# Kernel tuning notes

Hardware: AMD Instinct MI355X
Metric: run time of the kernel (lower is better)

## Reference

```python
import jax, jax.numpy as jnp
import numpy as np

N = 20000
E = 320000
F_IN = 256
NHID = 64
H1 = 8
H2 = 1
NUM_CLASSES = 40
NEG_SLOPE = 0.2


def setup_inputs() -> dict:
    key = jax.random.key(0)
    ks = jax.random.split(key, 11)
    glorot = lambda k, shape: jax.random.normal(k, shape, jnp.float32) * jnp.sqrt(2.0 / (shape[0] + shape[-1]))
    x = jax.random.normal(ks[0], (N, F_IN), jnp.float32)
    edge_index = jax.random.randint(ks[1], (2, E), 0, N, jnp.int64)
    W1 = glorot(ks[2], (F_IN, H1 * NHID))
    att_src1 = glorot(ks[3], (H1, NHID))
    att_dst1 = glorot(ks[4], (H1, NHID))
    b1 = jnp.zeros((H1 * NHID,), jnp.float32)
    W2 = glorot(ks[5], (H1 * NHID, H2 * NUM_CLASSES))
    att_src2 = glorot(ks[6], (H2, NUM_CLASSES))
    att_dst2 = glorot(ks[7], (H2, NUM_CLASSES))
    b2 = jnp.zeros((NUM_CLASSES,), jnp.float32)
    return {"x": x, "edge_index": edge_index, "W1": W1, "att_src1": att_src1,
            "att_dst1": att_dst1, "b1": b1, "W2": W2, "att_src2": att_src2,
            "att_dst2": att_dst2, "b2": b2}


def gat_conv(x, src, dst, W, a_src, a_dst, bias, concat):
    # x: [N, F_in], src/dst: [E'] (self-loops already appended)
    H, C = a_src.shape
    h = (x @ W).reshape(N, H, C)                       # [N,H,C]
    alpha_src = jnp.sum(h * a_src, axis=-1)            # [N,H]
    alpha_dst = jnp.sum(h * a_dst, axis=-1)            # [N,H]
    e = jax.nn.leaky_relu(alpha_src[src] + alpha_dst[dst], NEG_SLOPE)  # [E',H]
    # segment softmax over incoming edges of each dst node
    emax = jax.lax.stop_gradient(jax.ops.segment_max(e, dst, num_segments=N))
    ee = jnp.exp(e - emax[dst])
    denom = jax.ops.segment_sum(ee, dst, num_segments=N)
    alpha = ee / (denom[dst] + 1e-16)                  # [E',H]
    out = jax.ops.segment_sum(alpha[:, :, None] * h[src], dst, num_segments=N)  # [N,H,C]
    out = out.reshape(N, H * C) if concat else out.mean(axis=1)
    return out + bias


def reference(x, edge_index, W1, att_src1, att_dst1, b1, W2, att_src2, att_dst2, b2):
    # PyG GATConv adds self-loops by default
    loops = jnp.arange(N, dtype=edge_index.dtype)
    src = jnp.concatenate([edge_index[0], loops])
    dst = jnp.concatenate([edge_index[1], loops])
    h = gat_conv(x, src, dst, W1, att_src1, att_dst1, b1, concat=True)   # [N, H1*NHID]
    h = jax.nn.elu(h)
    out = gat_conv(h, src, dst, W2, att_src2, att_dst2, b2, concat=False)  # [N, NUM_CLASSES]
    return jax.nn.log_softmax(out, axis=1)
```

## Files before the change

kernel.cpp:

```cpp
#include <hip/hip_runtime.h>
#include <hip/hip_bf16.h>
#include <math.h>

#define N_NODES 20000
#define MPAD 20096
#define N_EDGES 320000
#define EP (N_EDGES + N_NODES)
#define F_IN 256
#define NHID 64
#define H1 8
#define D1 512
#define NCLS 40
#define NEG_SLOPE 0.2f
#define MAXD 128

typedef __attribute__((ext_vector_type(8))) short bf16x8;
typedef __attribute__((ext_vector_type(4))) float f32x4;

__device__ __forceinline__ float wave_max(float v) {
#pragma unroll
  for (int o = 32; o > 0; o >>= 1) v = fmaxf(v, __shfl_xor(v, o));
  return v;
}
__device__ __forceinline__ float wave_sum(float v) {
#pragma unroll
  for (int o = 32; o > 0; o >>= 1) v += __shfl_xor(v, o);
  return v;
}
__device__ __forceinline__ float bf2f(unsigned short u) {
  union { unsigned int i; float f; } c; c.i = ((unsigned int)u) << 16; return c.f;
}
__device__ __forceinline__ unsigned short f2bf(float f) {
  union { float f; unsigned int i; } c; c.f = f;
  unsigned int x = c.i;
  return (unsigned short)((x + 0x7fffu + ((x >> 16) & 1u)) >> 16);
}
__device__ __forceinline__ float asf(unsigned int u) {
  union { unsigned int i; float f; } c; c.i = u; return c.f;
}
__device__ __forceinline__ float lrelu(float x) { return x > 0.f ? x : NEG_SLOPE * x; }

__device__ __forceinline__ void gload16(const void* g, void* l) {
  __builtin_amdgcn_global_load_lds((const __attribute__((address_space(1))) void*)g,
                                   (__attribute__((address_space(3))) void*)l, 16, 0, 0);
}

#define PB_CONV 2512
#define PB_TW1  (PB_CONV + 32)
#define PB_TW2  (PB_TW1 + 96)
#define PB_ZERO (PB_TW2 + 157)
#define PB_PAD  (PB_ZERO + 24)
__global__ __launch_bounds__(256) void prep_kernel(const float* __restrict__ x,
                                                   const float* __restrict__ W1,
                                                   const float* __restrict__ W2,
                                                   unsigned short* __restrict__ xb,
                                                   unsigned short* __restrict__ wb1t,
                                                   unsigned short* __restrict__ wb2t,
                                                   int* __restrict__ deg,
                                                   int* __restrict__ cursor,
                                                   unsigned short* __restrict__ out1b) {
  __shared__ float tsh[64][65];
  int bid = blockIdx.x;
  int t = threadIdx.x;
  if (bid < PB_CONV) {
    size_t base = ((size_t)bid * 256 + t) * 8;
    int row = (int)(base >> 8);
    ushort4 o0, o1;
    if (row < N_NODES) {
      float4 v0 = *(const float4*)&x[base];
      float4 v1 = *(const float4*)&x[base + 4];
      o0 = make_ushort4(f2bf(v0.x), f2bf(v0.y), f2bf(v0.z), f2bf(v0.w));
      o1 = make_ushort4(f2bf(v1.x), f2bf(v1.y), f2bf(v1.z), f2bf(v1.w));
    } else {
      o0 = make_ushort4(0, 0, 0, 0); o1 = o0;
    }
    *(ushort4*)&xb[base] = o0;
    *(ushort4*)&xb[base + 4] = o1;
  } else if (bid < PB_TW1) {
    int b2 = bid - PB_CONV;
    int bk = b2 & 3, bn = b2 >> 2;
    int tr = t >> 4, tc4 = (t & 15) * 4;
#pragma unroll
    for (int i = 0; i < 4; ++i) {
      int k = i * 16 + tr;
      float4 v = *(const float4*)&W1[(size_t)(bk * 64 + k) * D1 + bn * 64 + tc4];
      tsh[k][tc4] = v.x; tsh[k][tc4 + 1] = v.y; tsh[k][tc4 + 2] = v.z; tsh[k][tc4 + 3] = v.w;
    }
    __syncthreads();
#pragma unroll
    for (int i = 0; i < 4; ++i) {
      int n = i * 16 + tr;
      ushort4 o = make_ushort4(f2bf(tsh[tc4][n]), f2bf(tsh[tc4 + 1][n]),
                               f2bf(tsh[tc4 + 2][n]), f2bf(tsh[tc4 + 3][n]));
      *(ushort4*)&wb1t[(size_t)(bn * 64 + n) * F_IN + bk * 64 + tc4] = o;
    }
  } else if (bid < PB_TW2) {
    int idx = (bid - PB_TW1) * 256 + t;
    int c = idx >> 9, k = idx & 511;
    wb2t[idx] = f2bf((c < NCLS) ? W2[(size_t)k * NCLS + c] : 0.f);
  } else if (bid < PB_ZERO) {
    int idx = (bid - PB_TW2) * 256 + t;
    if (idx < N_NODES) deg[idx] = 0;
    else if (idx < 2 * N_NODES) cursor[idx - N_NODES] = 0;
  } else {
    int idx = (bid - PB_ZERO) * 256 + t;
    uint4 z = make_uint4(0, 0, 0, 0);
    *(uint4*)((char*)out1b + (size_t)N_NODES * D1 * 2 + (size_t)idx * 16) = z;
  }
}

__global__ void count_deg(const int* __restrict__ ei, int* __restrict__ deg) {
  int e = blockIdx.x * blockDim.x + threadIdx.x;
  if (e >= EP) return;
  int dst = (e < N_EDGES) ? ei[N_EDGES + e] : (e - N_EDGES);
  atomicAdd(&deg[dst], 1);
}

#define SCAN_T 1024
#define SCAN_CHUNK 20
__global__ __launch_bounds__(1024) void scan_kernel(const int* __restrict__ deg,
                                                    int* __restrict__ offsets) {
  __shared__ int wsum[16];
  int t = threadIdx.x;
  int w = t >> 6, lane = t & 63;
  int lo = t * SCAN_CHUNK;
  int hi = min(lo + SCAN_CHUNK, N_NODES);
  int s = 0;
  for (int i = lo; i < hi; ++i) s += deg[i];
  int incl = s;
#pragma unroll
  for (int o = 1; o < 64; o <<= 1) {
    int v = __shfl_up(incl, o);
    if (lane >= o) incl += v;
  }
  if (lane == 63) wsum[w] = incl;
  __syncthreads();
  if (t == 0) {
    int run = 0;
#pragma unroll
    for (int i = 0; i < 16; ++i) { int v = wsum[i]; wsum[i] = run; run += v; }
  }
  __syncthreads();
  int off = wsum[w] + incl - s;
  for (int i = lo; i < hi; ++i) { offsets[i] = off; off += deg[i]; }
  if (hi == N_NODES && lo < N_NODES) offsets[N_NODES] = off;
}

__global__ void scatter_edges(const int* __restrict__ ei, const int* __restrict__ offsets,
                              int* __restrict__ cursor, int* __restrict__ edge_src) {
  int e = blockIdx.x * blockDim.x + threadIdx.x;
  if (e >= EP) return;
  int src, dst;
  if (e < N_EDGES) { src = ei[e]; dst = ei[N_EDGES + e]; }
  else             { src = dst = e - N_EDGES; }
  int pos = offsets[dst] + atomicAdd(&cursor[dst], 1);
  edge_src[pos] = src;
}

__global__ __launch_bounds__(256) void gemm1_mfma(const unsigned short* __restrict__ xb,
                                                  const unsigned short* __restrict__ wb1t,
                                                  const float* __restrict__ a_src,
                                                  const float* __restrict__ a_dst,
                                                  unsigned short* __restrict__ h1b,
                                                  float* __restrict__ asrc,
                                                  float* __restrict__ adst) {
  __shared__ unsigned short As[128 * 64];
  __shared__ unsigned short Bs[128 * 64];
  int tid = threadIdx.x;
  int w = tid >> 6, lane = tid & 63;
  int bn = blockIdx.x & 3, bm = blockIdx.x >> 2;
  int row0 = bm * 128, col0 = bn * 128;
  int wr = w >> 1, wc = w & 1;
  int cl = lane & 15, hi = lane >> 4;
  f32x4 acc[4][4] = {};
  for (int k0 = 0; k0 < F_IN; k0 += 64) {
#pragma unroll
    for (int c = 0; c < 4; ++c) {
      int slot = c * 256 + tid;
      int r = slot >> 3;
      int q = (slot & 7) ^ (r & 7);
      gload16(xb + (size_t)(row0 + r) * F_IN + k0 + q * 8, (char*)As + (c * 256 + w * 64) * 16);
      gload16(wb1t + (size_t)(col0 + r) * F_IN + k0 + q * 8, (char*)Bs + (c * 256 + w * 64) * 16);
    }
    __syncthreads();
#pragma unroll
    for (int kk = 0; kk < 2; ++kk) {
      bf16x8 a[4], b[4];
#pragma unroll
      for (int m = 0; m < 4; ++m) {
        int r = wr * 64 + m * 16 + cl;
        a[m] = *(const bf16x8*)&As[r * 64 + ((((kk * 4 + hi)) ^ (r & 7)) << 3)];
      }
#pragma unroll
      for (int n = 0; n < 4; ++n) {
        int r = wc * 64 + n * 16 + cl;
        b[n] = *(const bf16x8*)&Bs[r * 64 + ((((kk * 4 + hi)) ^ (r & 7)) << 3)];
      }
#pragma unroll
      for (int m = 0; m < 4; ++m)
#pragma unroll
        for (int n = 0; n < 4; ++n)
          acc[m][n] = __builtin_amdgcn_mfma_f32_16x16x32_bf16(a[m], b[n], acc[m][n], 0, 0, 0);
    }
    __syncthreads();
  }
  int head = bn * 2 + wc;
  float asv[4], adv[4];
#pragma unroll
  for (int n = 0; n < 4; ++n) {
    asv[n] = a_src[head * 64 + n * 16 + cl];
    adv[n] = a_dst[head * 64 + n * 16 + cl];
  }
#pragma unroll
  for (int m = 0; m < 4; ++m) {
#pragma unroll
    for (int r = 0; r < 4; ++r) {
      int grow = row0 + wr * 64 + m * 16 + hi * 4 + r;
      float ps = acc[m][0][r] * asv[0] + acc[m][1][r] * asv[1] +
                 acc[m][2][r] * asv[2] + acc[m][3][r] * asv[3];
      float pd = acc[m][0][r] * adv[0] + acc[m][1][r] * adv[1] +
                 acc[m][2][r] * adv[2] + acc[m][3][r] * adv[3];
#pragma unroll
      for (int o = 8; o > 0; o >>= 1) { ps += __shfl_xor(ps, o); pd += __shfl_xor(pd, o); }
      if (grow < N_NODES) {
#pragma unroll
        for (int n = 0; n < 4; ++n)
          h1b[(size_t)grow * D1 + col0 + wc * 64 + n * 16 + cl] = f2bf(acc[m][n][r]);
        if (cl == 0) { asrc[grow * H1 + head] = ps; adst[grow * H1 + head] = pd; }
      }
    }
  }
}

__global__ __launch_bounds__(256) void agg1_kernel(const int* __restrict__ offsets,
                                                   const int* __restrict__ edge_src,
                                                   const float* __restrict__ asrc,
                                                   const float* __restrict__ adst,
                                                   const unsigned short* __restrict__ h1b,
                                                   const float* __restrict__ b1,
                                                   unsigned short* __restrict__ out1b) {
  __shared__ float alphaT[4][MAXD][H1];
  __shared__ int   lsoff[4][MAXD];
  int w = threadIdx.x >> 6, lane = threadIdx.x & 63;
  int n = blockIdx.x * 4 + w;
  int base = offsets[n];
  int deg = offsets[n + 1] - base;
  int degc = min(deg, MAXD);

  for (int e = lane; e < degc; e += 64) lsoff[w][e] = edge_src[base + e] << 10;
  __builtin_amdgcn_wave_barrier();

  int h = lane & 7, et = lane >> 3;
  float advv = adst[n * H1 + h];
  float m = -INFINITY;
  for (int e = et; e < degc; e += 8) {
    int s = lsoff[w][e] >> 10;
    float ev = lrelu(asrc[s * H1 + h] + advv);
    alphaT[w][e][h] = ev;
    m = fmaxf(m, ev);
  }
  for (int e = MAXD + et; e < deg; e += 8)
    m = fmaxf(m, lrelu(asrc[edge_src[base + e] * H1 + h] + advv));
  m = fmaxf(m, __shfl_xor(m, 8));
  m = fmaxf(m, __shfl_xor(m, 16));
  m = fmaxf(m, __shfl_xor(m, 32));
  float ss = 0.f;
  for (int e = et; e < degc; e += 8) ss += __expf(alphaT[w][e][h] - m);
  for (int e = MAXD + et; e < deg; e += 8)
    ss += __expf(lrelu(asrc[edge_src[base + e] * H1 + h] + advv) - m);
  ss += __shfl_xor(ss, 8);
  ss += __shfl_xor(ss, 16);
  ss += __shfl_xor(ss, 32);
  float inv = 1.f / (ss + 1e-16f);
  for (int e = et; e < degc; e += 8)
    alphaT[w][e][h] = __expf(alphaT[w][e][h] - m) * inv;
  __builtin_amdgcn_wave_barrier();

  int myh = lane >> 3;
  const char* hb = (const char*)h1b + lane * 16;
  float acc[8] = {};
  int e = 0;
  for (; e + 1 < degc; e += 2) {
    float a0 = alphaT[w][e][myh];
    float a1 = alphaT[w][e + 1][myh];
    uint4 u0 = *(const uint4*)(hb + lsoff[w][e]);
    uint4 u1 = *(const uint4*)(hb + lsoff[w][e + 1]);
#pragma unroll
    for (int j = 0; j < 4; ++j) {
      unsigned int x0 = ((const unsigned int*)&u0)[j];
      unsigned int x1 = ((const unsigned int*)&u1)[j];
      acc[2 * j]     += a0 * asf(x0 << 16);
      acc[2 * j + 1] += a0 * asf(x0 & 0xffff0000u);
      acc[2 * j]     += a1 * asf(x1 << 16);
      acc[2 * j + 1] += a1 * asf(x1 & 0xffff0000u);
    }
  }
  for (; e < degc; ++e) {
    float a = alphaT[w][e][myh];
    uint4 uv = *(const uint4*)(hb + lsoff[w][e]);
#pragma unroll
    for (int j = 0; j < 4; ++j) {
      unsigned int u = ((const unsigned int*)&uv)[j];
      acc[2 * j]     += a * asf(u << 16);
      acc[2 * j + 1] += a * asf(u & 0xffff0000u);
    }
  }
  if (deg > MAXD) {
    float mh = __shfl(m, myh);
    float invh = __shfl(inv, myh);
    float advh = adst[n * H1 + myh];
    for (int e2 = MAXD; e2 < deg; ++e2) {
      int s = edge_src[base + e2];
      float a = __expf(lrelu(asrc[s * H1 + myh] + advh) - mh) * invh;
      uint4 uv = *(const uint4*)(hb + ((size_t)s << 10));
#pragma unroll
      for (int j = 0; j < 4; ++j) {
        unsigned int u = ((const unsigned int*)&uv)[j];
        acc[2 * j]     += a * asf(u << 16);
        acc[2 * j + 1] += a * asf(u & 0xffff0000u);
      }
    }
  }

  int c0 = lane * 8;
  float4 b0 = *(const float4*)&b1[c0];
  float4 b4 = *(const float4*)&b1[c0 + 4];
  float v[8];
  v[0] = acc[0] + b0.x; v[1] = acc[1] + b0.y; v[2] = acc[2] + b0.z; v[3] = acc[3] + b0.w;
  v[4] = acc[4] + b4.x; v[5] = acc[5] + b4.y; v[6] = acc[6] + b4.z; v[7] = acc[7] + b4.w;
#pragma unroll
  for (int j = 0; j < 8; ++j) v[j] = v[j] > 0.f ? v[j] : (__expf(v[j]) - 1.f);
  ushort4 o0 = make_ushort4(f2bf(v[0]), f2bf(v[1]), f2bf(v[2]), f2bf(v[3]));
  ushort4 o1 = make_ushort4(f2bf(v[4]), f2bf(v[5]), f2bf(v[6]), f2bf(v[7]));
  *(ushort4*)&out1b[(size_t)n * D1 + c0] = o0;
  *(ushort4*)&out1b[(size_t)n * D1 + c0 + 4] = o1;
}

__global__ __launch_bounds__(256) void gemm2_mfma(const unsigned short* __restrict__ ab,
                                                  const unsigned short* __restrict__ wb2t,
                                                  const float* __restrict__ a_src2,
                                                  const float* __restrict__ a_dst2,
                                                  float* __restrict__ h2,
                                                  float* __restrict__ asrc,
                                                  float* __restrict__ adst) {
  __shared__ unsigned short As[64 * 64];
  __shared__ unsigned short Bs[48 * 64];
  int tid = threadIdx.x;
  int w = tid >> 6, lane = tid & 63;
  int row0 = blockIdx.x * 64;
  int cl = lane & 15, hi = lane >> 4;
  f32x4 acc[3] = {};
  for (int k0 = 0; k0 < D1; k0 += 64) {
#pragma unroll
    for (int c = 0; c < 2; ++c) {
      int slot = c * 256 + tid;
      int r = slot >> 3;
      int q = (slot & 7) ^ (r & 7);
      gload16(ab + (size_t)(row0 + r) * D1 + k0 + q * 8, (char*)As + (c * 256 + w * 64) * 16);
    }
    {
      int r = tid >> 3;
      int q = (tid & 7) ^ (r & 7);
      gload16(wb2t + (size_t)r * D1 + k0 + q * 8, (char*)Bs + (w * 64) * 16);
      if (tid < 128) {
        int slot2 = 256 + tid;
        int r2 = slot2 >> 3;
        int q2 = (slot2 & 7) ^ (r2 & 7);
        gload16(wb2t + (size_t)r2 * D1 + k0 + q2 * 8, (char*)Bs + ((256 + w * 64)) * 16);
      }
    }
    __syncthreads();
#pragma unroll
    for (int kk = 0; kk < 2; ++kk) {
      int ra = w * 16 + cl;
      bf16x8 a = *(const bf16x8*)&As[ra * 64 + (((kk * 4 + hi) ^ (ra & 7)) << 3)];
#pragma unroll
      for (int n = 0; n < 3; ++n) {
        int rb = n * 16 + cl;
        bf16x8 b = *(const bf16x8*)&Bs[rb * 64 + (((kk * 4 + hi) ^ (rb & 7)) << 3)];
        acc[n] = __builtin_amdgcn_mfma_f32_16x16x32_bf16(a, b, acc[n], 0, 0, 0);
      }
    }
    __syncthreads();
  }
  float asv[3], adv[3];
#pragma unroll
  for (int n = 0; n < 3; ++n) {
    int c = n * 16 + cl;
    asv[n] = (c < NCLS) ? a_src2[c] : 0.f;
    adv[n] = (c < NCLS) ? a_dst2[c] : 0.f;
  }
#pragma unroll
  for (int r = 0; r < 4; ++r) {
    int grow = row0 + w * 16 + hi * 4 + r;
    float ps = acc[0][r] * asv[0] + acc[1][r] * asv[1] + acc[2][r] * asv[2];
    float pd = acc[0][r] * adv[0] + acc[1][r] * adv[1] + acc[2][r] * adv[2];
#pragma unroll
    for (int o = 8; o > 0; o >>= 1) { ps += __shfl_xor(ps, o); pd += __shfl_xor(pd, o); }
    if (grow < N_NODES) {
#pragma unroll
      for (int n = 0; n < 3; ++n) {
        int c = n * 16 + cl;
        if (c < NCLS) h2[(size_t)grow * NCLS + c] = acc[n][r];
      }
      if (cl == 0) { asrc[grow] = ps; adst[grow] = pd; }
    }
  }
}

__global__ __launch_bounds__(256) void agg2_kernel(const int* __restrict__ offsets,
                                                   const int* __restrict__ edge_src,
                                                   const float* __restrict__ asrc,
                                                   const float* __restrict__ adst,
                                                   const float* __restrict__ h2,
                                                   const float* __restrict__ b2,
                                                   float* __restrict__ out) {
  __shared__ float lalpha[4][MAXD];
  __shared__ int   lsoff[4][MAXD];
  int w = threadIdx.x >> 6;
  int lane = threadIdx.x & 63;
  int n = blockIdx.x * 4 + w;
  int base = offsets[n];
  int deg = offsets[n + 1] - base;
  int degc = min(deg, MAXD);
  int degp = ((degc + 2) / 3) * 3;

  float advv = adst[n];
  float m = -INFINITY;
  for (int e = lane; e < deg; e += 64) {
    int s = edge_src[base + e];
    float ev = lrelu(asrc[s] + advv);
    if (e < MAXD) { lsoff[w][e] = s * (NCLS * 4); lalpha[w][e] = ev; }
    m = fmaxf(m, ev);
  }
  m = wave_max(m);
  float ssum = 0.f;
  for (int e = lane; e < deg; e += 64) {
    float ev;
    if (e < MAXD) ev = lalpha[w][e];
    else { int s = edge_src[base + e]; ev = lrelu(asrc[s] + advv); }
    ssum += __expf(ev - m);
  }
  float inv = 1.f / (wave_sum(ssum) + 1e-16f);
  for (int e = lane; e < degc; e += 64) lalpha[w][e] = __expf(lalpha[w][e] - m) * inv;
  {
    int e = degc + lane;
    if (e < degp && e < MAXD) { lalpha[w][e] = 0.f; lsoff[w][e] = 0; }
  }
  __builtin_amdgcn_wave_barrier();

  int esub = lane / 20;
  int cg = lane - esub * 20;
  bool act = esub < 3;
  float ax = 0.f, ay = 0.f;
  const char* hb = (const char*)h2 + cg * 8;
  for (int i = 0; i < degp; i += 3) {
    if (act) {
      int slot = i + esub;
      float a = lalpha[w][slot];
      int so = lsoff[w][slot];
      float2 hv = *(const float2*)(hb + so);
      ax += a * hv.x; ay += a * hv.y;
    }
  }
  for (int e = MAXD + esub; e < deg; e += 3) {
    if (act) {
      int s = edge_src[base + e];
      float a = __expf(lrelu(asrc[s] + advv) - m) * inv;
      float2 hv = *(const float2*)(hb + (size_t)s * (NCLS * 4));
      ax += a * hv.x; ay += a * hv.y;
    }
  }
  float ax1 = __shfl(ax, lane + 20), ax2 = __shfl(ax, lane + 40);
  float ay1 = __shfl(ay, lane + 20), ay2 = __shfl(ay, lane + 40);
  float v0 = -INFINITY, v1 = -INFINITY;
  if (lane < 20) {
    v0 = ax + ax1 + ax2 + b2[2 * cg];
    v1 = ay + ay1 + ay2 + b2[2 * cg + 1];
  }
  float m2 = wave_max(fmaxf(v0, v1));
  float se = wave_sum(lane < 20 ? __expf(v0 - m2) + __expf(v1 - m2) : 0.f);
  if (lane < 20) {
    float ls = logf(se);
    *(float2*)&out[(size_t)n * NCLS + 2 * cg] = make_float2(v0 - m2 - ls, v1 - m2 - ls);
  }
}

extern "C" void kernel_launch(void* const* d_in, const int* in_sizes, int n_in,
                              void* d_out, int out_size, void* d_ws, size_t ws_size,
                              hipStream_t stream) {
  const float* x   = (const float*)d_in[0];
  const int*   ei  = (const int*)d_in[1];
  const float* W1  = (const float*)d_in[2];
  const float* as1 = (const float*)d_in[3];
  const float* ad1 = (const float*)d_in[4];
  const float* b1  = (const float*)d_in[5];
  const float* W2  = (const float*)d_in[6];
  const float* as2 = (const float*)d_in[7];
  const float* ad2 = (const float*)d_in[8];
  const float* b2  = (const float*)d_in[9];
  float* out = (float*)d_out;

  char* ws = (char*)d_ws;
  size_t off = 0;
  auto alloc = [&](size_t bytes) -> char* {
    char* p = ws + off;
    off += (bytes + 255) & ~(size_t)255;
    return p;
  };
  int* deg      = (int*)alloc((size_t)N_NODES * 4);
  int* cursor   = (int*)alloc((size_t)N_NODES * 4);
  int* offsets  = (int*)alloc((size_t)(N_NODES + 1) * 4);
  int* edge_src = (int*)alloc((size_t)EP * 4);
  unsigned short* xb    = (unsigned short*)alloc((size_t)MPAD * F_IN * 2);
  unsigned short* wb1t  = (unsigned short*)alloc((size_t)D1 * F_IN * 2);
  unsigned short* wb2t  = (unsigned short*)alloc((size_t)48 * D1 * 2);
  unsigned short* h1b   = (unsigned short*)alloc((size_t)N_NODES * D1 * 2);
  unsigned short* out1b = (unsigned short*)alloc((size_t)MPAD * D1 * 2);
  float* asrc1  = (float*)alloc((size_t)N_NODES * H1 * 4);
  float* adst1  = (float*)alloc((size_t)N_NODES * H1 * 4);
  float* h2     = (float*)alloc((size_t)N_NODES * NCLS * 4);
  float* asrc2  = (float*)alloc((size_t)N_NODES * 4);
  float* adst2  = (float*)alloc((size_t)N_NODES * 4);

  prep_kernel<<<PB_PAD, 256, 0, stream>>>(x, W1, W2, xb, wb1t, wb2t, deg, cursor, out1b);
  count_deg<<<(EP + 255) / 256, 256, 0, stream>>>(ei, deg);
  scan_kernel<<<1, SCAN_T, 0, stream>>>(deg, offsets);
  scatter_edges<<<(EP + 255) / 256, 256, 0, stream>>>(ei, offsets, cursor, edge_src);

  gemm1_mfma<<<157 * 4, 256, 0, stream>>>(xb, wb1t, as1, ad1, h1b, asrc1, adst1);
  agg1_kernel<<<N_NODES / 4, 256, 0, stream>>>(offsets, edge_src, asrc1, adst1, h1b, b1, out1b);

  gemm2_mfma<<<MPAD / 64, 256, 0, stream>>>(out1b, wb2t, as2, ad2, h2, asrc2, adst2);
  agg2_kernel<<<N_NODES / 4, 256, 0, stream>>>(offsets, edge_src, asrc2, adst2, h2, b2, out);
}
```

Measured before the change: 159.3 us.

## Split layer-1 aggregation across heads with one wave per node-head pair

The layer-1 aggregation kernel now launches eight times more blocks, and each wave handles a single (node, head) pair instead of all eight heads of one node. Softmax values for up to 64 edges live in registers and are broadcast with shuffles, which replaces the shared-memory alpha and offset tables. The gather processes four edges at a time with 8-byte loads per lane, followed by a cross-lane reduction. This raises parallelism and removes LDS use, at the cost of re-reading offsets, edge_src and asrc once per head, issuing narrower gather loads, and leaving most lanes idle for low-degree nodes.

After: 192.2 us. +20.6%, slower.

```diff
diff --git a/kernel.cpp b/kernel.cpp
--- a/kernel.cpp
+++ b/kernel.cpp
@@ -239,101 +239,71 @@
                                                    const unsigned short* __restrict__ h1b,
                                                    const float* __restrict__ b1,
                                                    unsigned short* __restrict__ out1b) {
-  __shared__ float alphaT[4][MAXD][H1];
-  __shared__ int   lsoff[4][MAXD];
   int w = threadIdx.x >> 6, lane = threadIdx.x & 63;
-  int n = blockIdx.x * 4 + w;
+  int bid = blockIdx.x;
+  int head = bid & 7;
+  int n = (bid >> 3) * 4 + w;
   int base = offsets[n];
   int deg = offsets[n + 1] - base;
-  int degc = min(deg, MAXD);
-
-  for (int e = lane; e < degc; e += 64) lsoff[w][e] = edge_src[base + e] << 10;
-  __builtin_amdgcn_wave_barrier();
-
-  int h = lane & 7, et = lane >> 3;
-  float advv = adst[n * H1 + h];
-  float m = -INFINITY;
-  for (int e = et; e < degc; e += 8) {
-    int s = lsoff[w][e] >> 10;
-    float ev = lrelu(asrc[s * H1 + h] + advv);
-    alphaT[w][e][h] = ev;
-    m = fmaxf(m, ev);
-  }
-  for (int e = MAXD + et; e < deg; e += 8)
-    m = fmaxf(m, lrelu(asrc[edge_src[base + e] * H1 + h] + advv));
-  m = fmaxf(m, __shfl_xor(m, 8));
-  m = fmaxf(m, __shfl_xor(m, 16));
-  m = fmaxf(m, __shfl_xor(m, 32));
-  float ss = 0.f;
-  for (int e = et; e < degc; e += 8) ss += __expf(alphaT[w][e][h] - m);
-  for (int e = MAXD + et; e < deg; e += 8)
-    ss += __expf(lrelu(asrc[edge_src[base + e] * H1 + h] + advv) - m);
-  ss += __shfl_xor(ss, 8);
-  ss += __shfl_xor(ss, 16);
-  ss += __shfl_xor(ss, 32);
-  float inv = 1.f / (ss + 1e-16f);
-  for (int e = et; e < degc; e += 8)
-    alphaT[w][e][h] = __expf(alphaT[w][e][h] - m) * inv;
-  __builtin_amdgcn_wave_barrier();
-
-  int myh = lane >> 3;
-  const char* hb = (const char*)h1b + lane * 16;
-  float acc[8] = {};
-  int e = 0;
-  for (; e + 1 < degc; e += 2) {
-    float a0 = alphaT[w][e][myh];
-    float a1 = alphaT[w][e + 1][myh];
-    uint4 u0 = *(const uint4*)(hb + lsoff[w][e]);
-    uint4 u1 = *(const uint4*)(hb + lsoff[w][e + 1]);
-#pragma unroll
-    for (int j = 0; j < 4; ++j) {
-      unsigned int x0 = ((const unsigned int*)&u0)[j];
-      unsigned int x1 = ((const unsigned int*)&u1)[j];
-      acc[2 * j]     += a0 * asf(x0 << 16);
-      acc[2 * j + 1] += a0 * asf(x0 & 0xffff0000u);
-      acc[2 * j]     += a1 * asf(x1 << 16);
-      acc[2 * j + 1] += a1 * asf(x1 & 0xffff0000u);
-    }
-  }
-  for (; e < degc; ++e) {
-    float a = alphaT[w][e][myh];
-    uint4 uv = *(const uint4*)(hb + lsoff[w][e]);
-#pragma unroll
-    for (int j = 0; j < 4; ++j) {
-      unsigned int u = ((const unsigned int*)&uv)[j];
-      acc[2 * j]     += a * asf(u << 16);
-      acc[2 * j + 1] += a * asf(u & 0xffff0000u);
-    }
-  }
-  if (deg > MAXD) {
-    float mh = __shfl(m, myh);
-    float invh = __shfl(inv, myh);
-    float advh = adst[n * H1 + myh];
-    for (int e2 = MAXD; e2 < deg; ++e2) {
-      int s = edge_src[base + e2];
-      float a = __expf(lrelu(asrc[s * H1 + myh] + advh) - mh) * invh;
-      uint4 uv = *(const uint4*)(hb + ((size_t)s << 10));
-#pragma unroll
-      for (int j = 0; j < 4; ++j) {
-        unsigned int u = ((const unsigned int*)&uv)[j];
-        acc[2 * j]     += a * asf(u << 16);
-        acc[2 * j + 1] += a * asf(u & 0xffff0000u);
-      }
-    }
-  }
-
-  int c0 = lane * 8;
-  float4 b0 = *(const float4*)&b1[c0];
-  float4 b4 = *(const float4*)&b1[c0 + 4];
-  float v[8];
-  v[0] = acc[0] + b0.x; v[1] = acc[1] + b0.y; v[2] = acc[2] + b0.z; v[3] = acc[3] + b0.w;
-  v[4] = acc[4] + b4.x; v[5] = acc[5] + b4.y; v[6] = acc[6] + b4.z; v[7] = acc[7] + b4.w;
-#pragma unroll
-  for (int j = 0; j < 8; ++j) v[j] = v[j] > 0.f ? v[j] : (__expf(v[j]) - 1.f);
-  ushort4 o0 = make_ushort4(f2bf(v[0]), f2bf(v[1]), f2bf(v[2]), f2bf(v[3]));
-  ushort4 o1 = make_ushort4(f2bf(v[4]), f2bf(v[5]), f2bf(v[6]), f2bf(v[7]));
-  *(ushort4*)&out1b[(size_t)n * D1 + c0] = o0;
-  *(ushort4*)&out1b[(size_t)n * D1 + c0 + 4] = o1;
+
+  float adv = adst[n * H1 + head];
+  int src = 0;
+  float ev = -INFINITY;
+  if (lane < deg) {
+    src = edge_src[base + lane];
+    ev = lrelu(asrc[src * H1 + head] + adv);
+  }
+  float mx = -INFINITY;
+  for (int e = 64 + lane; e < deg; e += 64)
+    mx = fmaxf(mx, lrelu(asrc[edge_src[base + e] * H1 + head] + adv));
+  float m = wave_max(fmaxf(ev, mx));
+  float ssl = (lane < deg) ? __expf(ev - m) : 0.f;
+  for (int e = 64 + lane; e < deg; e += 64)
+    ssl += __expf(lrelu(asrc[edge_src[base + e] * H1 + head] + adv) - m);
+  float inv = 1.f / (wave_sum(ssl) + 1e-16f);
+  float alpha = (lane < deg) ? __expf(ev - m) * inv : 0.f;
+  int rowoff = src << 10;
+
+  int eg = lane >> 4, cl = lane & 15;
+  const char* hb = (const char*)h1b + head * 128 + cl * 8;
+  float a0 = 0.f, a1 = 0.f, a2 = 0.f, a3 = 0.f;
+  int dc = min(deg, 64);
+  for (int e0 = 0; e0 < dc; e0 += 4) {
+    int e = e0 + eg;
+    int esafe = (e < dc) ? e : 0;
+    float a = __shfl(alpha, esafe);
+    int ro = __shfl(rowoff, esafe);
+    if (e >= dc) a = 0.f;
+    uint2 uv = *(const uint2*)(hb + ro);
+    a0 += a * asf(uv.x << 16);
+    a1 += a * asf(uv.x & 0xffff0000u);
+    a2 += a * asf(uv.y << 16);
+    a3 += a * asf(uv.y & 0xffff0000u);
+  }
+  for (int e = 64 + eg; e < deg; e += 4) {
+    int s2 = edge_src[base + e];
+    float a = __expf(lrelu(asrc[s2 * H1 + head] + adv) - m) * inv;
+    uint2 uv = *(const uint2*)(hb + ((size_t)s2 << 10));
+    a0 += a * asf(uv.x << 16);
+    a1 += a * asf(uv.x & 0xffff0000u);
+    a2 += a * asf(uv.y << 16);
+    a3 += a * asf(uv.y & 0xffff0000u);
+  }
+  a0 += __shfl_xor(a0, 16); a0 += __shfl_xor(a0, 32);
+  a1 += __shfl_xor(a1, 16); a1 += __shfl_xor(a1, 32);
+  a2 += __shfl_xor(a2, 16); a2 += __shfl_xor(a2, 32);
+  a3 += __shfl_xor(a3, 16); a3 += __shfl_xor(a3, 32);
+  if (lane < 16) {
+    int c0 = head * NHID + cl * 4;
+    float4 bv = *(const float4*)&b1[c0];
+    float v0 = a0 + bv.x, v1 = a1 + bv.y, v2 = a2 + bv.z, v3 = a3 + bv.w;
+    v0 = v0 > 0.f ? v0 : (__expf(v0) - 1.f);
+    v1 = v1 > 0.f ? v1 : (__expf(v1) - 1.f);
+    v2 = v2 > 0.f ? v2 : (__expf(v2) - 1.f);
+    v3 = v3 > 0.f ? v3 : (__expf(v3) - 1.f);
+    ushort4 o = make_ushort4(f2bf(v0), f2bf(v1), f2bf(v2), f2bf(v3));
+    *(ushort4*)&out1b[(size_t)n * D1 + c0] = o;
+  }
 }
 
 __global__ __launch_bounds__(256) void gemm2_mfma(const unsigned short* __restrict__ ab,
@@ -529,7 +499,7 @@
   scatter_edges<<<(EP + 255) / 256, 256, 0, stream>>>(ei, offsets, cursor, edge_src);
 
   gemm1_mfma<<<157 * 4, 256, 0, stream>>>(xb, wb1t, as1, ad1, h1b, asrc1, adst1);
-  agg1_kernel<<<N_NODES / 4, 256, 0, stream>>>(offsets, edge_src, asrc1, adst1, h1b, b1, out1b);
+  agg1_kernel<<<(N_NODES / 4) * 8, 256, 0, stream>>>(offsets, edge_src, asrc1, adst1, h1b, b1, out1b);
 
   gemm2_mfma<<<MPAD / 64, 256, 0, stream>>>(out1b, wb2t, as2, ad2, h2, asrc2, adst2);
   agg2_kernel<<<N_NODES / 4, 256, 0, stream>>>(offsets, edge_src, asrc2, adst2, h2, b2, out);
```

## Split layer-1 aggregation into per-edge alpha kernel and head-parallel gather

Applied to the files above, without the earlier changes.

Layer-1 aggregation is split in two. A new kernel computes the unnormalized attention exponentials per edge and head, writes them to a head-major global array, and stores each node's inverse softmax sum. A second kernel gathers features with one 8-lane group per node and one head per block, so blocks grouped by head touch a 128-byte slice of h1 rows, and normalization moves to the epilogue. This drops the LDS staging and the MAXD special path, but adds an extra launch and a global round trip for roughly 11 MB of alpha values. It also reloads edge_src once per head.

Result: no change. 162.5 us (+2.0%).

```diff
diff --git a/kernel.cpp b/kernel.cpp
--- a/kernel.cpp
+++ b/kernel.cpp
@@ -26,9 +26,6 @@
 #pragma unroll
   for (int o = 32; o > 0; o >>= 1) v += __shfl_xor(v, o);
   return v;
-}
-__device__ __forceinline__ float bf2f(unsigned short u) {
-  union { unsigned int i; float f; } c; c.i = ((unsigned int)u) << 16; return c.f;
 }
 __device__ __forceinline__ unsigned short f2bf(float f) {
   union { float f; unsigned int i; } c; c.f = f;
@@ -232,72 +229,91 @@
   }
 }
 
-__global__ __launch_bounds__(256) void agg1_kernel(const int* __restrict__ offsets,
-                                                   const int* __restrict__ edge_src,
-                                                   const float* __restrict__ asrc,
-                                                   const float* __restrict__ adst,
-                                                   const unsigned short* __restrict__ h1b,
-                                                   const float* __restrict__ b1,
-                                                   unsigned short* __restrict__ out1b) {
-  __shared__ float alphaT[4][MAXD][H1];
-  __shared__ int   lsoff[4][MAXD];
+__global__ __launch_bounds__(256) void alpha1_kernel(const int* __restrict__ offsets,
+                                                     const int* __restrict__ edge_src,
+                                                     const float* __restrict__ asrc,
+                                                     const float* __restrict__ adst,
+                                                     float* __restrict__ alphaE,
+                                                     float* __restrict__ inv1) {
   int w = threadIdx.x >> 6, lane = threadIdx.x & 63;
   int n = blockIdx.x * 4 + w;
   int base = offsets[n];
   int deg = offsets[n + 1] - base;
-  int degc = min(deg, MAXD);
-
-  for (int e = lane; e < degc; e += 64) lsoff[w][e] = edge_src[base + e] << 10;
-  __builtin_amdgcn_wave_barrier();
-
   int h = lane & 7, et = lane >> 3;
-  float advv = adst[n * H1 + h];
+  float adv = adst[n * H1 + h];
+  float evr[8];
   float m = -INFINITY;
-  for (int e = et; e < degc; e += 8) {
-    int s = lsoff[w][e] >> 10;
-    float ev = lrelu(asrc[s * H1 + h] + advv);
-    alphaT[w][e][h] = ev;
+#pragma unroll
+  for (int k = 0; k < 8; ++k) {
+    int e = et + k * 8;
+    float ev = -INFINITY;
+    if (e < deg) ev = lrelu(asrc[edge_src[base + e] * H1 + h] + adv);
+    evr[k] = ev;
     m = fmaxf(m, ev);
   }
-  for (int e = MAXD + et; e < deg; e += 8)
-    m = fmaxf(m, lrelu(asrc[edge_src[base + e] * H1 + h] + advv));
+  for (int e = et + 64; e < deg; e += 8)
+    m = fmaxf(m, lrelu(asrc[edge_src[base + e] * H1 + h] + adv));
   m = fmaxf(m, __shfl_xor(m, 8));
   m = fmaxf(m, __shfl_xor(m, 16));
   m = fmaxf(m, __shfl_xor(m, 32));
   float ss = 0.f;
-  for (int e = et; e < degc; e += 8) ss += __expf(alphaT[w][e][h] - m);
-  for (int e = MAXD + et; e < deg; e += 8)
-    ss += __expf(lrelu(asrc[edge_src[base + e] * H1 + h] + advv) - m);
+#pragma unroll
+  for (int k = 0; k < 8; ++k) {
+    int e = et + k * 8;
+    if (e < deg) {
+      float a = __expf(evr[k] - m);
+      alphaE[(size_t)h * EP + base + e] = a;
+      ss += a;
+    }
+  }
+  for (int e = et + 64; e < deg; e += 8) {
+    float a = __expf(lrelu(asrc[edge_src[base + e] * H1 + h] + adv) - m);
+    alphaE[(size_t)h * EP + base + e] = a;
+    ss += a;
+  }
   ss += __shfl_xor(ss, 8);
   ss += __shfl_xor(ss, 16);
   ss += __shfl_xor(ss, 32);
-  float inv = 1.f / (ss + 1e-16f);
-  for (int e = et; e < degc; e += 8)
-    alphaT[w][e][h] = __expf(alphaT[w][e][h] - m) * inv;
-  __builtin_amdgcn_wave_barrier();
-
-  int myh = lane >> 3;
-  const char* hb = (const char*)h1b + lane * 16;
+  if (et == 0) inv1[n * H1 + h] = 1.f / (ss + 1e-16f);
+}
+
+__global__ __launch_bounds__(256) void agg1_gather(const int* __restrict__ offsets,
+                                                   const int* __restrict__ edge_src,
+                                                   const float* __restrict__ alphaE,
+                                                   const float* __restrict__ inv1,
+                                                   const unsigned short* __restrict__ h1b,
+                                                   const float* __restrict__ b1,
+                                                   unsigned short* __restrict__ out1b) {
+  int w = threadIdx.x >> 6, lane = threadIdx.x & 63;
+  int bid = blockIdx.x;
+  int head = bid & 7;
+  int ng = bid >> 3;
+  int sub = lane >> 3, cl = lane & 7;
+  int n = ng * 32 + w * 8 + sub;
+  int base = offsets[n];
+  int deg = offsets[n + 1] - base;
+  const float* aE = alphaE + (size_t)head * EP + base;
+  const int* es = edge_src + base;
+  const char* hb = (const char*)h1b + head * 128 + cl * 16;
   float acc[8] = {};
   int e = 0;
-  for (; e + 1 < degc; e += 2) {
-    float a0 = alphaT[w][e][myh];
-    float a1 = alphaT[w][e + 1][myh];
-    uint4 u0 = *(const uint4*)(hb + lsoff[w][e]);
-    uint4 u1 = *(const uint4*)(hb + lsoff[w][e + 1]);
+  for (; e + 1 < deg; e += 2) {
+    float a0 = aE[e], a1 = aE[e + 1];
+    int s0 = es[e], s1 = es[e + 1];
+    uint4 u0 = *(const uint4*)(hb + ((size_t)s0 << 10));
+    uint4 u1 = *(const uint4*)(hb + ((size_t)s1 << 10));
 #pragma unroll
     for (int j = 0; j < 4; ++j) {
       unsigned int x0 = ((const unsigned int*)&u0)[j];
       unsigned int x1 = ((const unsigned int*)&u1)[j];
-      acc[2 * j]     += a0 * asf(x0 << 16);
-      acc[2 * j + 1] += a0 * asf(x0 & 0xffff0000u);
-      acc[2 * j]     += a1 * asf(x1 << 16);
-      acc[2 * j + 1] += a1 * asf(x1 & 0xffff0000u);
-    }
-  }
-  for (; e < degc; ++e) {
-    float a = alphaT[w][e][myh];
-    uint4 uv = *(const uint4*)(hb + lsoff[w][e]);
+      acc[2 * j]     += a0 * asf(x0 << 16) + a1 * asf(x1 << 16);
+      acc[2 * j + 1] += a0 * asf(x0 & 0xffff0000u) + a1 * asf(x1 & 0xffff0000u);
+    }
+  }
+  if (e < deg) {
+    float a = aE[e];
+    int s = es[e];
+    uint4 uv = *(const uint4*)(hb + ((size_t)s << 10));
 #pragma unroll
     for (int j = 0; j < 4; ++j) {
       unsigned int u = ((const unsigned int*)&uv)[j];
@@ -305,29 +321,15 @@
       acc[2 * j + 1] += a * asf(u & 0xffff0000u);
     }
   }
-  if (deg > MAXD) {
-    float mh = __shfl(m, myh);
-    float invh = __shfl(inv, myh);
-    float advh = adst[n * H1 + myh];
-    for (int e2 = MAXD; e2 < deg; ++e2) {
-      int s = edge_src[base + e2];
-      float a = __expf(lrelu(asrc[s * H1 + myh] + advh) - mh) * invh;
-      uint4 uv = *(const uint4*)(hb + ((size_t)s << 10));
-#pragma unroll
-      for (int j = 0; j < 4; ++j) {
-        unsigned int u = ((const unsigned int*)&uv)[j];
-        acc[2 * j]     += a * asf(u << 16);
-        acc[2 * j + 1] += a * asf(u & 0xffff0000u);
-      }
-    }
-  }
-
-  int c0 = lane * 8;
+  float inv = inv1[n * H1 + head];
+  int c0 = head * NHID + cl * 8;
   float4 b0 = *(const float4*)&b1[c0];
   float4 b4 = *(const float4*)&b1[c0 + 4];
   float v[8];
-  v[0] = acc[0] + b0.x; v[1] = acc[1] + b0.y; v[2] = acc[2] + b0.z; v[3] = acc[3] + b0.w;
-  v[4] = acc[4] + b4.x; v[5] = acc[5] + b4.y; v[6] = acc[6] + b4.z; v[7] = acc[7] + b4.w;
+  v[0] = acc[0] * inv + b0.x; v[1] = acc[1] * inv + b0.y;
+  v[2] = acc[2] * inv + b0.z; v[3] = acc[3] * inv + b0.w;
+  v[4] = acc[4] * inv + b4.x; v[5] = acc[5] * inv + b4.y;
+  v[6] = acc[6] * inv + b4.z; v[7] = acc[7] * inv + b4.w;
 #pragma unroll
   for (int j = 0; j < 8; ++j) v[j] = v[j] > 0.f ? v[j] : (__expf(v[j]) - 1.f);
   ushort4 o0 = make_ushort4(f2bf(v[0]), f2bf(v[1]), f2bf(v[2]), f2bf(v[3]));
@@ -519,6 +521,8 @@
   unsigned short* out1b = (unsigned short*)alloc((size_t)MPAD * D1 * 2);
   float* asrc1  = (float*)alloc((size_t)N_NODES * H1 * 4);
   float* adst1  = (float*)alloc((size_t)N_NODES * H1 * 4);
+  float* alphaE = (float*)alloc((size_t)H1 * EP * 4);
+  float* inv1   = (float*)alloc((size_t)N_NODES * H1 * 4);
   float* h2     = (float*)alloc((size_t)N_NODES * NCLS * 4);
   float* asrc2  = (float*)alloc((size_t)N_NODES * 4);
   float* adst2  = (float*)alloc((size_t)N_NODES * 4);
@@ -529,7 +533,8 @@
   scatter_edges<<<(EP + 255) / 256, 256, 0, stream>>>(ei, offsets, cursor, edge_src);
 
   gemm1_mfma<<<157 * 4, 256, 0, stream>>>(xb, wb1t, as1, ad1, h1b, asrc1, adst1);
-  agg1_kernel<<<N_NODES / 4, 256, 0, stream>>>(offsets, edge_src, asrc1, adst1, h1b, b1, out1b);
+  alpha1_kernel<<<N_NODES / 4, 256, 0, stream>>>(offsets, edge_src, asrc1, adst1, alphaE, inv1);
+  agg1_gather<<<(N_NODES / 32) * 8, 256, 0, stream>>>(offsets, edge_src, alphaE, inv1, h1b, b1, out1b);
 
   gemm2_mfma<<<MPAD / 64, 256, 0, stream>>>(out1b, wb2t, as2, ad2, h2, asrc2, adst2);
   agg2_kernel<<<N_NODES / 4, 256, 0, stream>>>(offsets, edge_src, asrc2, adst2, h2, b2, out);
```
